# Kernel tuning notes

Measured on AMD Instinct MI355X. Metric: run time of the kernel, lower is better.

## Reference

```python
import jax, jax.numpy as jnp
import numpy as np

G, N, F_IN, D, R, E, L = 512, 128, 64, 128, 4, 1572864, 2  # graphs, nodes/graph, in-feat, embed, relations, edges, gnn layers


def setup_inputs() -> dict:
    key = jax.random.key(0)
    ks = jax.random.split(key, 8)
    x = jax.random.normal(ks[0], (G * N, F_IN), jnp.float32)
    # edges are within-graph (disjoint batched graph, as built by batch_to_gd)
    gid = jax.random.randint(ks[1], (E,), 0, G)
    loc = jax.random.randint(ks[2], (2, E), 0, N)
    edge_index = gid[None, :] * N + loc  # [2, E] (src, dst)
    edge_attr = jax.random.randint(ks[3], (E,), 0, R)
    W_emb = jax.random.normal(ks[4], (F_IN, D), jnp.float32) / np.sqrt(F_IN)
    b_emb = jnp.zeros((D,), jnp.float32)
    W_root = jax.random.normal(ks[5], (L, D, D), jnp.float32) / np.sqrt(D)
    W_rel = jax.random.normal(ks[6], (L, R, D, D), jnp.float32) / np.sqrt(D)
    bias = jnp.zeros((L, D), jnp.float32)
    return {"x": x, "edge_index": edge_index, "edge_attr": edge_attr,
            "W_emb": W_emb, "b_emb": b_emb, "W_root": W_root, "W_rel": W_rel, "bias": bias}


def rgcn_layer(h, edge_index, edge_attr, W_root_l, W_rel_l, bias_l):
    # PyG RGCNConv: out_i = h_i @ W_root + sum_r mean_{j in N_r(i)} (h_j @ W_r) + bias
    n = h.shape[0]
    xr = jnp.einsum('nd,rde->rne', h, W_rel_l)          # [R, n, D] per-relation transform
    src, dst = edge_index[0], edge_index[1]
    msg = xr[edge_attr, src]                             # [E, D] gather per edge
    seg = dst * R + edge_attr                            # combined (node, relation) segment id
    summed = jax.ops.segment_sum(msg, seg, num_segments=n * R)
    cnt = jax.ops.segment_sum(jnp.ones((msg.shape[0],), h.dtype), seg, num_segments=n * R)
    mean = summed / jnp.maximum(cnt, 1.0)[:, None]       # per-relation mean aggregation
    agg = mean.reshape(n, R, -1).sum(axis=1)             # sum over relations
    return h @ W_root_l + agg + bias_l


def reference(x, edge_index, edge_attr, W_emb, b_emb, W_root, W_rel, bias):
    h = x @ W_emb + b_emb                                # embedding_linear
    for l in range(L):                                   # mp_rounds = 1 per layer
        h = jax.nn.relu(rgcn_layer(h, edge_index, edge_attr, W_root[l], W_rel[l], bias[l]))
    # split into per-graph chunks of N nodes and max-pool over nodes
    return jnp.max(h.reshape(G, N, -1), axis=1)          # [G, D]
```

## Files before the change

kernel.cpp:

```cpp
#include <hip/hip_runtime.h>

constexpr int GG    = 512;
constexpr int NPG   = 128;
constexpr int FIN   = 64;
constexpr int DD    = 128;
constexpr int RR    = 4;
constexpr int NN    = GG * NPG;
constexpr int EE    = 1572864;
constexpr int SLC   = 4096;
constexpr int HSTR  = 136;

typedef __attribute__((ext_vector_type(8))) short bf16x8;
typedef __attribute__((ext_vector_type(4))) float f32x4;
typedef __attribute__((ext_vector_type(2))) float f32x2;
typedef unsigned short u16;
typedef unsigned int   u32;

__device__ __forceinline__ u32 bf16_rne(float x) {
    u32 u = __float_as_uint(x);
    return (u + 0x7FFFu + ((u >> 16) & 1u)) >> 16;
}

__device__ __forceinline__ void gl_lds16(const void* g, void* l) {
    __builtin_amdgcn_global_load_lds((const __attribute__((address_space(1))) u32*)g,
                                     (__attribute__((address_space(3))) u32*)l, 16, 0, 0);
}


__global__ __launch_bounds__(256, 2) void k_front(const int* __restrict__ ei,
                                                  const int* __restrict__ ea,
                                                  u32* __restrict__ bcur,
                                                  u16* __restrict__ binned,
                                                  const float* __restrict__ W_root,
                                                  const float* __restrict__ W_rel,
                                                  const float* __restrict__ W_emb,
                                                  u16* __restrict__ wtH) {
    __shared__ u32 sRec[4096];
    __shared__ int bh[512];
    __shared__ int lcur[512];
    __shared__ float tile[32 * 129];
    int tid = threadIdx.x;
    int bid = blockIdx.x;

    if (bid < 384) {
        int e0 = bid * 4096;
        bh[tid] = 0; bh[tid + 256] = 0;
        __syncthreads();
        for (int i = 0; i < 16; ++i) {
            int e = e0 + i * 256 + tid;
            int src = ei[e];
            int dst = ei[EE + e];
            int a   = ea[e];
            int g   = dst >> 7;
            u32 rec = (u32)(src & 127) | ((u32)(dst & 127) << 7) | ((u32)a << 14);
            sRec[i * 256 + tid] = rec | ((u32)g << 16);
            atomicAdd(&bh[g], 1);
        }
        __syncthreads();
        lcur[tid]       = tid * SLC +
                          (int)atomicAdd(&bcur[tid], (u32)bh[tid]);
        lcur[tid + 256] = (tid + 256) * SLC +
                          (int)atomicAdd(&bcur[tid + 256], (u32)bh[tid + 256]);
        __syncthreads();
        for (int i = 0; i < 16; ++i) {
            u32 r = sRec[i * 256 + tid];
            int pos = atomicAdd(&lcur[r >> 16], 1);
            binned[pos] = (u16)(r & 0xFFFFu);
        }
    } else if (bid < 424) {
        int pb = bid - 384;
        int mat = pb >> 2;
        int k0 = (pb & 3) * 32;
        int l = mat / 5, m5 = mat - l * 5;
        const float* Wsrc = (m5 == 0) ? (W_root + l * 16384)
                                      : (W_rel + (size_t)(l * RR + (m5 - 1)) * 16384);
        for (int i = 0; i < 16; ++i) {
            int k = k0 + (tid >> 7) + i * 2;
            int n = tid & 127;
            tile[(k - k0) * 129 + n] = Wsrc[k * 128 + n];
        }
        __syncthreads();
        for (int i = 0; i < 16; ++i) {
            int kk = tid & 31;
            int n  = (tid >> 5) + i * 8;
            wtH[mat * 16384 + n * 128 + k0 + kk] = (u16)bf16_rne(tile[kk * 129 + n]);
        }
    } else {
        int k0 = (bid - 424) * 32;
        for (int i = 0; i < 16; ++i) {
            int k = k0 + (tid >> 7) + i * 2;
            int n = tid & 127;
            tile[(k - k0) * 129 + n] = W_emb[k * 128 + n];
        }
        __syncthreads();
        for (int i = 0; i < 16; ++i) {
            int kk = tid & 31;
            int n  = (tid >> 5) + i * 8;
            wtH[163840 + n * 64 + k0 + kk] = (u16)bf16_rne(tile[kk * 129 + n]);
        }
    }
}


__global__ __launch_bounds__(512, 4) void k_fused(const float* __restrict__ x,
                                                  const float* __restrict__ b_emb,
                                                  float* __restrict__ outF,
                                                  const u16* __restrict__ wtH,
                                                  const float* __restrict__ bias,
                                                  const u16* __restrict__ binned,
                                                  const u32* __restrict__ bcur) {
    __shared__ __align__(16) u16 hG[128 * HSTR];
    __shared__ __align__(16) u16 sQ[2][4096];
    __shared__ u16   sIdx[SLC];
    __shared__ int   sOffs[513];
    __shared__ int   sCnt[512];
    __shared__ float sInv[512];
    __shared__ float red[8][128];

    int tid  = threadIdx.x;
    int wave = tid >> 6, lane = tid & 63;
    int mm   = lane & 15;
    int qd   = lane >> 4;
    int gr   = blockIdx.x;
    int row0g = gr * NPG;
    int strip = wave * 16;
    const u16* wtE = wtH + 163840;

    auto stage = [&](int step, int bufi) {
        const u16* src = wtH + (step >> 2) * 16384 + (step & 3) * 32;
        int u = tid;
        int n = u >> 2, j = u & 3;
        gl_lds16(src + n * 128 + ((j ^ ((n >> 1) & 3)) * 8), &sQ[bufi][u * 8]);
    };
    auto stageE = [&](int q, int bufi) {
        const u16* src = wtE + q * 32;
        int u = tid;
        int n = u >> 2, j = u & 3;
        gl_lds16(src + n * 64 + ((j ^ ((n >> 1) & 3)) * 8), &sQ[bufi][u * 8]);
    };

    f32x4 acc[8];
    auto mfma_quarter = [&](int bufi, bf16x8 A) {
        const u16* buf = sQ[bufi];
#pragma unroll
        for (int nt = 0; nt < 8; ++nt) {
            int n = nt * 16 + mm;
            int slot = n * 4 + (qd ^ ((n >> 1) & 3));
            bf16x8 B = *(const bf16x8*)&buf[slot * 8];
            acc[nt] = __builtin_amdgcn_mfma_f32_16x16x32_bf16(A, B, acc[nt], 0, 0, 0);
        }
    };

    auto gather = [&](int rel, bf16x8* AH) {
        int key = (rel << 7) + strip + mm;
        int r0 = sOffs[key];
        int r1 = sOffs[key + 1];
        float s = sInv[key];
#pragma unroll
        for (int h = 0; h < 2; ++h) {
            int cb = h * 64 + qd * 8;
            f32x2 ax[8];
#pragma unroll
            for (int i = 0; i < 8; ++i) ax[i] = (f32x2){0.f, 0.f};
            auto upk8 = [&](int ks, uint4 u) {
                ax[ks*4+0] += (f32x2){__uint_as_float(u.x << 16),
                                      __uint_as_float(u.x & 0xffff0000u)};
                ax[ks*4+1] += (f32x2){__uint_as_float(u.y << 16),
                                      __uint_as_float(u.y & 0xffff0000u)};
                ax[ks*4+2] += (f32x2){__uint_as_float(u.z << 16),
                                      __uint_as_float(u.z & 0xffff0000u)};
                ax[ks*4+3] += (f32x2){__uint_as_float(u.w << 16),
                                      __uint_as_float(u.w & 0xffff0000u)};
            };
            int j = r0;
            for (; j + 2 <= r1; j += 2) {
                int rb0 = (int)sIdx[j]     * HSTR + cb;
                int rb1 = (int)sIdx[j + 1] * HSTR + cb;
                uint4 a0 = *(const uint4*)&hG[rb0];
                uint4 a1 = *(const uint4*)&hG[rb0 + 32];
                uint4 b0 = *(const uint4*)&hG[rb1];
                uint4 b1 = *(const uint4*)&hG[rb1 + 32];
                upk8(0, a0); upk8(1, a1); upk8(0, b0); upk8(1, b1);
            }
            if (j < r1) {
                int rb = (int)sIdx[j] * HSTR + cb;
                uint4 a0 = *(const uint4*)&hG[rb];
                uint4 a1 = *(const uint4*)&hG[rb + 32];
                upk8(0, a0); upk8(1, a1);
            }
#pragma unroll
            for (int k2 = 0; k2 < 2; ++k2) {
                uint4 u;
                u.x = bf16_rne(ax[k2*4+0].x * s) | (bf16_rne(ax[k2*4+0].y * s) << 16);
                u.y = bf16_rne(ax[k2*4+1].x * s) | (bf16_rne(ax[k2*4+1].y * s) << 16);
                u.z = bf16_rne(ax[k2*4+2].x * s) | (bf16_rne(ax[k2*4+2].y * s) << 16);
                u.w = bf16_rne(ax[k2*4+3].x * s) | (bf16_rne(ax[k2*4+3].y * s) << 16);
                AH[h * 2 + k2] = *(bf16x8*)&u;
            }
        }
    };

    stageE(0, 0);
    int cnt = (int)bcur[gr];
    if (cnt > SLC) cnt = SLC;
    uint4 myRec = *(const uint4*)&binned[gr * SLC + tid * 8];
    sCnt[tid] = 0;
    __syncthreads();
    int base8 = tid * 8;
#pragma unroll
    for (int i = 0; i < 8; ++i) {
        if (base8 + i < cnt) {
            u32 w = ((const u32*)&myRec)[i >> 1];
            u32 rec = (i & 1) ? (w >> 16) : (w & 0xFFFFu);
            atomicAdd(&sCnt[rec >> 7], 1);
        }
    }
    __syncthreads();
    int c = sCnt[tid];
    sOffs[tid] = c;
    __syncthreads();
    for (int o = 1; o < 512; o <<= 1) {
        int t = (tid >= o) ? sOffs[tid - o] : 0;
        __syncthreads();
        sOffs[tid] += t;
        __syncthreads();
    }
    int ex = sOffs[tid] - c;
    sOffs[tid] = ex;
    sCnt[tid]  = ex;
    sInv[tid]  = 1.0f / (float)(c > 0 ? c : 1);
    if (tid == 0) sOffs[512] = cnt;
    __syncthreads();
#pragma unroll
    for (int i = 0; i < 8; ++i) {
        if (base8 + i < cnt) {
            u32 w = ((const u32*)&myRec)[i >> 1];
            u32 rec = (i & 1) ? (w >> 16) : (w & 0xFFFFu);
            int pos = atomicAdd(&sCnt[rec >> 7], 1);
            sIdx[pos] = (u16)(rec & 127u);
        }
    }
    __syncthreads();

    {
#pragma unroll
        for (int nt = 0; nt < 8; ++nt) {
            float bv = b_emb[nt * 16 + mm];
            acc[nt] = (f32x4){bv, bv, bv, bv};
        }
        bf16x8 AE[2];
#pragma unroll
        for (int ks = 0; ks < 2; ++ks) {
            const float* xp = &x[(size_t)(row0g + strip + mm) * FIN + ks * 32 + qd * 8];
            float4 a = *(const float4*)xp;
            float4 b = *(const float4*)(xp + 4);
            uint4 u;
            u.x = bf16_rne(a.x) | (bf16_rne(a.y) << 16);
            u.y = bf16_rne(a.z) | (bf16_rne(a.w) << 16);
            u.z = bf16_rne(b.x) | (bf16_rne(b.y) << 16);
            u.w = bf16_rne(b.z) | (bf16_rne(b.w) << 16);
            AE[ks] = *(bf16x8*)&u;
        }
        stageE(1, 1);
        mfma_quarter(0, AE[0]);
        __syncthreads();
        stage(0, 0);
        mfma_quarter(1, AE[1]);
        __syncthreads();
#pragma unroll
        for (int nt = 0; nt < 8; ++nt)
#pragma unroll
            for (int r = 0; r < 4; ++r)
                hG[(strip + qd * 4 + r) * HSTR + nt * 16 + mm] =
                    (u16)bf16_rne(acc[nt][r]);
        __syncthreads();
    }

    for (int L = 0; L < 2; ++L) {
        const float* bl = bias + L * DD;
#pragma unroll
        for (int i = 0; i < 8; ++i) acc[i] = (f32x4){0.f, 0.f, 0.f, 0.f};

        bf16x8 AH[4];
#pragma unroll
        for (int ks = 0; ks < 4; ++ks)
            AH[ks] = *(const bf16x8*)&hG[(strip + mm) * HSTR + ks * 32 + qd * 8];

        for (int m = 0; m < 5; ++m) {
#pragma unroll
            for (int q = 0; q < 4; ++q) {
                int step = L * 20 + m * 4 + q;
                if (step + 1 < 40) stage(step + 1, (step + 1) & 1);
                mfma_quarter(step & 1, AH[q]);
                __syncthreads();
            }
            if (m < 4) gather(m, AH);
        }

        if (L == 0) {
#pragma unroll
            for (int nt = 0; nt < 8; ++nt) {
                float bv = bl[nt * 16 + mm];
#pragma unroll
                for (int r = 0; r < 4; ++r)
                    hG[(strip + qd * 4 + r) * HSTR + nt * 16 + mm] =
                        (u16)bf16_rne(fmaxf(acc[nt][r] + bv, 0.f));
            }
            __syncthreads();
        } else {
#pragma unroll
            for (int nt = 0; nt < 8; ++nt) {
                float bv = bl[nt * 16 + mm];
                float v = fmaxf(fmaxf(acc[nt][0], acc[nt][1]),
                                fmaxf(acc[nt][2], acc[nt][3])) + bv;
                v = fmaxf(v, 0.f);
                v = fmaxf(v, __shfl_xor(v, 16));
                v = fmaxf(v, __shfl_xor(v, 32));
                if (lane < 16) red[wave][nt * 16 + mm] = v;
            }
            __syncthreads();
            if (tid < 128) {
                float mx = red[0][tid];
#pragma unroll
                for (int w = 1; w < 8; ++w) mx = fmaxf(mx, red[w][tid]);
                outF[gr * DD + tid] = mx;
            }
        }
    }
}


extern "C" void kernel_launch(void* const* d_in, const int* in_sizes, int n_in,
                              void* d_out, int out_size, void* d_ws, size_t ws_size,
                              hipStream_t stream) {
    const float* x      = (const float*)d_in[0];
    const int*   ei     = (const int*)  d_in[1];
    const int*   ea     = (const int*)  d_in[2];
    const float* W_emb  = (const float*)d_in[3];
    const float* b_emb  = (const float*)d_in[4];
    const float* W_root = (const float*)d_in[5];
    const float* W_rel  = (const float*)d_in[6];
    const float* bias   = (const float*)d_in[7];
    float* out = (float*)d_out;

    char* p = (char*)d_ws;
    u32* bcur   = (u32*)p; p += 2048;
    u16* binned = (u16*)p; p += (size_t)GG * SLC * 2;
    u16* wtH    = (u16*)p; p += (size_t)(10 * 16384 + 8192) * 2;

    hipMemsetAsync(bcur, 0, 2048, stream);

    k_front<<<426, 256, 0, stream>>>(ei, ea, bcur, binned,
                                     W_root, W_rel, W_emb, wtH);
    k_fused<<<GG, 512, 0, stream>>>(x, b_emb, out, wtH, bias, binned, bcur);
}
```

Measured before the change: 188.4 us.

## Stage weights in half-K chunks and replace block scan with wave shuffle scan

The weight pipeline now stages 64-wide K halves per buffer with an 8-way XOR swizzle, so each stage-and-sync step issues two MFMAs per output tile and the number of barriers in the layer loop halves. The 512-entry block-wide Hillis-Steele prefix sum with many __syncthreads is replaced by a wave-level shuffle scan plus a small cross-wave combine, and sOffs[key+1] lookups now read the end offsets left in sCnt. The max-pool reduction buffer is aliased onto sIdx to offset the larger double buffer. LDS use per block grows, which may affect occupancy under launch_bounds(512,4).

```diff
diff --git a/kernel.cpp b/kernel.cpp
--- a/kernel.cpp
+++ b/kernel.cpp
@@ -110,12 +110,11 @@
                                                   const u16* __restrict__ binned,
                                                   const u32* __restrict__ bcur) {
     __shared__ __align__(16) u16 hG[128 * HSTR];
-    __shared__ __align__(16) u16 sQ[2][4096];
-    __shared__ u16   sIdx[SLC];
-    __shared__ int   sOffs[513];
+    __shared__ __align__(16) u16 sQ[2][8192];
+    __shared__ __align__(16) u16 sIdx[SLC];
+    __shared__ int   sOffs[512];
     __shared__ int   sCnt[512];
     __shared__ float sInv[512];
-    __shared__ float red[8][128];
 
     int tid  = threadIdx.x;
     int wave = tid >> 6, lane = tid & 63;
@@ -127,34 +126,44 @@
     const u16* wtE = wtH + 163840;
 
     auto stage = [&](int step, int bufi) {
-        const u16* src = wtH + (step >> 2) * 16384 + (step & 3) * 32;
-        int u = tid;
-        int n = u >> 2, j = u & 3;
-        gl_lds16(src + n * 128 + ((j ^ ((n >> 1) & 3)) * 8), &sQ[bufi][u * 8]);
+        const u16* src = wtH + (step >> 1) * 16384 + (step & 1) * 64;
+#pragma unroll
+        for (int i = 0; i < 2; ++i) {
+            int u = i * 512 + tid;
+            int n = u >> 3, j = u & 7;
+            gl_lds16(src + n * 128 + ((j ^ (n & 7)) * 8), &sQ[bufi][u * 8]);
+        }
     };
-    auto stageE = [&](int q, int bufi) {
-        const u16* src = wtE + q * 32;
-        int u = tid;
-        int n = u >> 2, j = u & 3;
-        gl_lds16(src + n * 64 + ((j ^ ((n >> 1) & 3)) * 8), &sQ[bufi][u * 8]);
+    auto stageE = [&](int bufi) {
+#pragma unroll
+        for (int i = 0; i < 2; ++i) {
+            int u = i * 512 + tid;
+            int n = u >> 3, j = u & 7;
+            gl_lds16(wtE + n * 64 + ((j ^ (n & 7)) * 8), &sQ[bufi][u * 8]);
+        }
     };
 
     f32x4 acc[8];
-    auto mfma_quarter = [&](int bufi, bf16x8 A) {
+    auto mfma_half = [&](int bufi, bf16x8 A0, bf16x8 A1) {
         const u16* buf = sQ[bufi];
 #pragma unroll
         for (int nt = 0; nt < 8; ++nt) {
             int n = nt * 16 + mm;
-            int slot = n * 4 + (qd ^ ((n >> 1) & 3));
-            bf16x8 B = *(const bf16x8*)&buf[slot * 8];
-            acc[nt] = __builtin_amdgcn_mfma_f32_16x16x32_bf16(A, B, acc[nt], 0, 0, 0);
+            int g0 = n * 8 + ((0 * 4 + qd) ^ (n & 7));
+            int g1 = n * 8 + ((1 * 4 + qd) ^ (n & 7));
+            bf16x8 B0 = *(const bf16x8*)&buf[g0 * 8];
+            bf16x8 B1 = *(const bf16x8*)&buf[g1 * 8];
+            f32x4 a = acc[nt];
+            a = __builtin_amdgcn_mfma_f32_16x16x32_bf16(A0, B0, a, 0, 0, 0);
+            a = __builtin_amdgcn_mfma_f32_16x16x32_bf16(A1, B1, a, 0, 0, 0);
+            acc[nt] = a;
         }
     };
 
     auto gather = [&](int rel, bf16x8* AH) {
         int key = (rel << 7) + strip + mm;
         int r0 = sOffs[key];
-        int r1 = sOffs[key + 1];
+        int r1 = sCnt[key];
         float s = sInv[key];
 #pragma unroll
         for (int h = 0; h < 2; ++h) {
@@ -200,7 +209,7 @@
         }
     };
 
-    stageE(0, 0);
+    stageE(0);
     int cnt = (int)bcur[gr];
     if (cnt > SLC) cnt = SLC;
     uint4 myRec = *(const uint4*)&binned[gr * SLC + tid * 8];
@@ -217,19 +226,25 @@
     }
     __syncthreads();
     int c = sCnt[tid];
-    sOffs[tid] = c;
-    __syncthreads();
-    for (int o = 1; o < 512; o <<= 1) {
-        int t = (tid >= o) ? sOffs[tid - o] : 0;
-        __syncthreads();
-        sOffs[tid] += t;
-        __syncthreads();
-    }
-    int ex = sOffs[tid] - c;
+    int v = c;
+#pragma unroll
+    for (int o = 1; o < 64; o <<= 1) {
+        int t = __shfl_up(v, o);
+        if (lane >= o) v += t;
+    }
+    int* wtot = (int*)sIdx;
+    if (lane == 63) wtot[wave] = v;
+    __syncthreads();
+    int base = 0;
+#pragma unroll
+    for (int w = 0; w < 8; ++w) {
+        int tw = wtot[w];
+        if (w < wave) base += tw;
+    }
+    int ex = base + v - c;
     sOffs[tid] = ex;
     sCnt[tid]  = ex;
     sInv[tid]  = 1.0f / (float)(c > 0 ? c : 1);
-    if (tid == 0) sOffs[512] = cnt;
     __syncthreads();
 #pragma unroll
     for (int i = 0; i < 8; ++i) {
@@ -261,12 +276,8 @@
             u.w = bf16_rne(b.z) | (bf16_rne(b.w) << 16);
             AE[ks] = *(bf16x8*)&u;
         }
-        stageE(1, 1);
-        mfma_quarter(0, AE[0]);
-        __syncthreads();
-        stage(0, 0);
-        mfma_quarter(1, AE[1]);
-        __syncthreads();
+        stage(0, 1);
+        mfma_half(0, AE[0], AE[1]);
 #pragma unroll
         for (int nt = 0; nt < 8; ++nt)
 #pragma unroll
@@ -288,10 +299,10 @@
 
         for (int m = 0; m < 5; ++m) {
 #pragma unroll
-            for (int q = 0; q < 4; ++q) {
-                int step = L * 20 + m * 4 + q;
-                if (step + 1 < 40) stage(step + 1, (step + 1) & 1);
-                mfma_quarter(step & 1, AH[q]);
+            for (int h = 0; h < 2; ++h) {
+                int s = L * 10 + m * 2 + h;
+                if (s + 1 < 20) stage(s + 1, s & 1);
+                mfma_half((s + 1) & 1, AH[h * 2], AH[h * 2 + 1]);
                 __syncthreads();
             }
             if (m < 4) gather(m, AH);
@@ -308,21 +319,22 @@
             }
             __syncthreads();
         } else {
+            float* red = (float*)sIdx;
 #pragma unroll
             for (int nt = 0; nt < 8; ++nt) {
                 float bv = bl[nt * 16 + mm];
-                float v = fmaxf(fmaxf(acc[nt][0], acc[nt][1]),
-                                fmaxf(acc[nt][2], acc[nt][3])) + bv;
-                v = fmaxf(v, 0.f);
-                v = fmaxf(v, __shfl_xor(v, 16));
-                v = fmaxf(v, __shfl_xor(v, 32));
-                if (lane < 16) red[wave][nt * 16 + mm] = v;
+                float vv = fmaxf(fmaxf(acc[nt][0], acc[nt][1]),
+                                 fmaxf(acc[nt][2], acc[nt][3])) + bv;
+                vv = fmaxf(vv, 0.f);
+                vv = fmaxf(vv, __shfl_xor(vv, 16));
+                vv = fmaxf(vv, __shfl_xor(vv, 32));
+                if (lane < 16) red[wave * 128 + nt * 16 + mm] = vv;
             }
             __syncthreads();
             if (tid < 128) {
-                float mx = red[0][tid];
-#pragma unroll
-                for (int w = 1; w < 8; ++w) mx = fmaxf(mx, red[w][tid]);
+                float mx = red[tid];
+#pragma unroll
+                for (int w = 1; w < 8; ++w) mx = fmaxf(mx, red[w * 128 + tid]);
                 outF[gr * DD + tid] = mx;
             }
         }
@@ -348,7 +360,7 @@
     u16* binned = (u16*)p; p += (size_t)GG * SLC * 2;
     u16* wtH    = (u16*)p; p += (size_t)(10 * 16384 + 8192) * 2;
 
-    hipMemsetAsync(bcur, 0, 2048, stream);
+    (void)hipMemsetAsync(bcur, 0, 2048, stream);
 
     k_front<<<426, 256, 0, stream>>>(ei, ea, bcur, binned,
                                      W_root, W_rel, W_emb, wtH);
```

Measured after the change: 184.3 us. 2.1% less time.
